# Kernel tuning notes

Hardware: AMD Instinct MI355X
Metric: run time of the kernel (lower is better)

Reference implementation:

```python
import jax, jax.numpy as jnp
import numpy as np

SEQ_LEN = 600
N_CLASSES = 5
P = 6  # max_ar_order


def setup_inputs() -> dict:
    key = jax.random.key(0)
    N = 32768
    x = jax.random.normal(key, (N, SEQ_LEN), dtype=jnp.float32)
    return {"x": x}


def reference(x):
    N = x.shape[0]
    T_out = SEQ_LEN - P
    # Lag matrix: X_lag[:, t, k] = x[:, P-1-k + t]  -> [N, T_out, P]
    X_lag = jnp.stack([x[:, P - 1 - k:SEQ_LEN - 1 - k] for k in range(P)], axis=-1)
    y = x[:, P:]  # [N, T_out]
    ones = jnp.ones((N, T_out, 1), dtype=x.dtype)
    D = jnp.concatenate([ones, X_lag], axis=-1)  # [N, T_out, P+1]
    # Least squares via normal equations (tiny (P+1)x(P+1) batched solve)
    G = jnp.einsum('ntk,ntl->nkl', D, D)        # [N, P+1, P+1]
    b = jnp.einsum('ntk,nt->nk', D, y)          # [N, P+1]
    w = jnp.linalg.solve(G, b[..., None])[..., 0]  # [N, P+1]
    y_hat_valid = jnp.einsum('ntk,nk->nt', D, w)   # [N, T_out]
    x_hat = jnp.zeros((N, SEQ_LEN), dtype=x.dtype).at[:, P:].set(y_hat_valid)
    ar_coeffs = w[:, 1:]  # [N, P]
    coeffs = jnp.broadcast_to(ar_coeffs[:, None, :], (N, SEQ_LEN, P))
    # zero the first P time steps
    t_mask = (jnp.arange(SEQ_LEN) >= P).astype(x.dtype)[None, :, None]
    coeffs = coeffs * t_mask
    p_logits = jnp.zeros((N, N_CLASSES), dtype=x.dtype)
    p_hard = jnp.zeros((N,), dtype=jnp.int32)
    return (coeffs, p_logits, p_hard, x_hat)
```

## Files before the change

kernel.cpp:

```cpp
#include <hip/hip_runtime.h>

#define SEQ 600
#define PP 6
#define TOUT 594

__global__ __launch_bounds__(256) void ar_fit_kernel(
    const float* __restrict__ x,
    float* __restrict__ coeffs,
    float* __restrict__ x_hat,
    int N)
{
    __shared__ __align__(16) float sxr[4][608];
    __shared__ float4 spat[4][3];

    const int wave = threadIdx.x >> 6;
    const int lane = threadIdx.x & 63;
    const int row  = (blockIdx.x << 2) + wave;
    const bool live = (row < N);

    if (live) {
        const float4* xr = reinterpret_cast<const float4*>(x + (size_t)row * SEQ);
        float4* s4 = reinterpret_cast<float4*>(sxr[wave]);
        for (int i = lane; i < SEQ / 4; i += 64) s4[i] = xr[i];
        if (lane < 8) sxr[wave][SEQ + lane] = 0.0f;
    }
    __syncthreads();

    const float* sx = sxr[wave];
    float w[7];

    if (live) {
        float S = 0.f;
        float Q[7] = {0.f, 0.f, 0.f, 0.f, 0.f, 0.f, 0.f};
        for (int i = lane; i < SEQ; i += 64) {
            float x0 = sx[i];
            S += x0;
            #pragma unroll
            for (int d = 0; d < 7; ++d) Q[d] += x0 * sx[i + d];
        }
        #pragma unroll
        for (int m = 1; m < 64; m <<= 1) {
            S += __shfl_xor(S, m, 64);
            #pragma unroll
            for (int d = 0; d < 7; ++d) Q[d] += __shfl_xor(Q[d], m, 64);
        }

        float pre[8], suf[8];
        pre[0] = 0.f; suf[0] = 0.f;
        #pragma unroll
        for (int c = 1; c < 8; ++c) {
            pre[c] = pre[c - 1] + sx[c - 1];
            suf[c] = suf[c - 1] + sx[SEQ - c];
        }

        float M[7][7];
        float rhs[7];
        M[0][0] = (float)TOUT;
        #pragma unroll
        for (int k = 0; k < 6; ++k) {
            float v = S - pre[5 - k] - suf[k + 1];
            M[0][k + 1] = v; M[k + 1][0] = v;
        }
        #pragma unroll
        for (int k = 0; k < 6; ++k) {
            #pragma unroll
            for (int l = k; l < 6; ++l) {
                const int a = 5 - l, d = l - k;
                float head = 0.f;
                #pragma unroll
                for (int i = 0; i < a; ++i) head += sx[i] * sx[i + d];
                float tail = 0.f;
                #pragma unroll
                for (int i = a + TOUT; i < SEQ; ++i) tail += sx[i] * sx[i + d];
                float v = Q[d] - head - tail;
                M[k + 1][l + 1] = v; M[l + 1][k + 1] = v;
            }
        }
        rhs[0] = S - pre[6];
        #pragma unroll
        for (int k = 0; k < 6; ++k) {
            const int a = 5 - k, d = k + 1;
            float head = 0.f;
            #pragma unroll
            for (int i = 0; i < a; ++i) head += sx[i] * sx[i + d];
            float tail = 0.f;
            #pragma unroll
            for (int i = a + TOUT; i < SEQ; ++i) tail += sx[i] * sx[i + d];
            rhs[k + 1] = Q[d] - head - tail;
        }

        #pragma unroll
        for (int j = 0; j < 7; ++j) {
            float s = M[j][j];
            #pragma unroll
            for (int m = 0; m < j; ++m) s -= M[j][m] * M[j][m];
            float ljj = sqrtf(s);
            M[j][j] = ljj;
            float inv = 1.0f / ljj;
            #pragma unroll
            for (int i2 = j + 1; i2 < 7; ++i2) {
                float s2 = M[i2][j];
                #pragma unroll
                for (int m = 0; m < j; ++m) s2 -= M[i2][m] * M[j][m];
                M[i2][j] = s2 * inv;
            }
        }
        float z[7];
        #pragma unroll
        for (int i2 = 0; i2 < 7; ++i2) {
            float s = rhs[i2];
            #pragma unroll
            for (int m = 0; m < i2; ++m) s -= M[i2][m] * z[m];
            z[i2] = s / M[i2][i2];
        }
        #pragma unroll
        for (int i2 = 6; i2 >= 0; --i2) {
            float s = z[i2];
            #pragma unroll
            for (int m = i2 + 1; m < 7; ++m) s -= M[m][i2] * w[m];
            w[i2] = s / M[i2][i2];
        }

        if (lane == 0) {
            float* p = reinterpret_cast<float*>(spat[wave]);
            #pragma unroll
            for (int m = 0; m < 12; ++m) p[m] = w[1 + (m % 6)];
        }
    }
    __syncthreads();

    if (!live) return;

    {
        float4* crow = reinterpret_cast<float4*>(coeffs + (size_t)row * (SEQ * PP));
        const float4* pw = spat[wave];
        int r = lane % 3;
        for (int i = lane; i < (SEQ * PP) / 4; i += 64) {
            float4 v = pw[r];
            if (i < 9) {
                float* vp = reinterpret_cast<float*>(&v);
                #pragma unroll
                for (int j = 0; j < 4; ++j)
                    if (4 * i + j < PP * PP) vp[j] = 0.f;
            }
            crow[i] = v;
            r = (r == 2) ? 0 : (r + 1);
        }
    }

    {
        float* xh = x_hat + (size_t)row * SEQ;
        for (int e = lane; e < SEQ; e += 64) {
            float v = 0.f;
            if (e >= PP) {
                v = w[0];
                #pragma unroll
                for (int k = 1; k <= 6; ++k) v += w[k] * sx[e - k];
            }
            xh[e] = v;
        }
    }
}

extern "C" void kernel_launch(void* const* d_in, const int* in_sizes, int n_in,
                              void* d_out, int out_size, void* d_ws, size_t ws_size,
                              hipStream_t stream) {
    const float* x = (const float*)d_in[0];
    const int N = in_sizes[0] / SEQ;

    float* out    = (float*)d_out;
    float* coeffs = out;
    float* extra  = out + (size_t)N * SEQ * PP;
    float* x_hat  = extra + (size_t)N * 6;

    hipMemsetAsync(extra, 0, (size_t)N * 6 * sizeof(float), stream);

    dim3 grid((N + 3) / 4), block(256);
    ar_fit_kernel<<<grid, block, 0, stream>>>(x, coeffs, x_hat, N);
}
```

Measured before the change: 594.2 us.

## Fuse memset into kernel, vectorize loads/stores with nontemporal writes

Zeroing of the logits/hard-label region moves into the main kernel, which removes the separate memset launch. Shared memory is read as float4, partial sums use register windows, and the coefficient and x_hat outputs are written with fully unrolled float4 nontemporal stores. The second __syncthreads and the shared pattern buffer are gone, divisions become hardware reciprocals, and the bounds checks are removed. The grid is now N/4, so N is assumed to be a multiple of 4.

```diff
diff --git a/kernel.cpp b/kernel.cpp
--- a/kernel.cpp
+++ b/kernel.cpp
@@ -3,161 +3,211 @@
 #define SEQ 600
 #define PP 6
 #define TOUT 594
-
-__global__ __launch_bounds__(256) void ar_fit_kernel(
+#define NF4 150
+#define NF4P 152
+
+typedef float v4f __attribute__((ext_vector_type(4)));
+
+__device__ __forceinline__ void nt_store4(float4* p, float4 v) {
+    v4f vv;
+    vv.x = v.x; vv.y = v.y; vv.z = v.z; vv.w = v.w;
+    __builtin_nontemporal_store(vv, reinterpret_cast<v4f*>(p));
+}
+
+__global__ __launch_bounds__(256) void ar_all_kernel(
     const float* __restrict__ x,
     float* __restrict__ coeffs,
+    float* __restrict__ extra,
     float* __restrict__ x_hat,
     int N)
 {
-    __shared__ __align__(16) float sxr[4][608];
-    __shared__ float4 spat[4][3];
+    __shared__ __align__(16) float4 sxr[4][NF4P];
 
     const int wave = threadIdx.x >> 6;
     const int lane = threadIdx.x & 63;
     const int row  = (blockIdx.x << 2) + wave;
-    const bool live = (row < N);
-
-    if (live) {
+
+    float4* s4 = sxr[wave];
+
+    {
         const float4* xr = reinterpret_cast<const float4*>(x + (size_t)row * SEQ);
-        float4* s4 = reinterpret_cast<float4*>(sxr[wave]);
-        for (int i = lane; i < SEQ / 4; i += 64) s4[i] = xr[i];
-        if (lane < 8) sxr[wave][SEQ + lane] = 0.0f;
+        float4 r0, r1, r2;
+        int m0 = lane, m1 = lane + 64, m2 = lane + 128;
+        r0 = xr[m0];
+        r1 = xr[m1];
+        if (m2 < NF4) r2 = xr[m2];
+        s4[m0] = r0;
+        s4[m1] = r1;
+        if (m2 < NF4) s4[m2] = r2;
+        if (lane < 2) s4[NF4 + lane] = make_float4(0.f, 0.f, 0.f, 0.f);
     }
     __syncthreads();
 
-    const float* sx = sxr[wave];
-    float w[7];
-
-    if (live) {
-        float S = 0.f;
-        float Q[7] = {0.f, 0.f, 0.f, 0.f, 0.f, 0.f, 0.f};
-        for (int i = lane; i < SEQ; i += 64) {
-            float x0 = sx[i];
-            S += x0;
-            #pragma unroll
-            for (int d = 0; d < 7; ++d) Q[d] += x0 * sx[i + d];
-        }
-        #pragma unroll
-        for (int m = 1; m < 64; m <<= 1) {
-            S += __shfl_xor(S, m, 64);
-            #pragma unroll
-            for (int d = 0; d < 7; ++d) Q[d] += __shfl_xor(Q[d], m, 64);
-        }
-
-        float pre[8], suf[8];
-        pre[0] = 0.f; suf[0] = 0.f;
-        #pragma unroll
-        for (int c = 1; c < 8; ++c) {
-            pre[c] = pre[c - 1] + sx[c - 1];
-            suf[c] = suf[c - 1] + sx[SEQ - c];
-        }
-
-        float M[7][7];
-        float rhs[7];
-        M[0][0] = (float)TOUT;
-        #pragma unroll
-        for (int k = 0; k < 6; ++k) {
-            float v = S - pre[5 - k] - suf[k + 1];
-            M[0][k + 1] = v; M[k + 1][0] = v;
-        }
-        #pragma unroll
-        for (int k = 0; k < 6; ++k) {
-            #pragma unroll
-            for (int l = k; l < 6; ++l) {
-                const int a = 5 - l, d = l - k;
-                float head = 0.f;
+    float S = 0.f;
+    float Q[7] = {0.f, 0.f, 0.f, 0.f, 0.f, 0.f, 0.f};
+    #pragma unroll
+    for (int k = 0; k < 3; ++k) {
+        const int m = lane + 64 * k;
+        if (m < NF4) {
+            float4 a = s4[m], b = s4[m + 1], c = s4[m + 2];
+            float W[12] = {a.x, a.y, a.z, a.w, b.x, b.y, b.z, b.w,
+                           c.x, c.y, c.z, c.w};
+            #pragma unroll
+            for (int cc = 0; cc < 4; ++cc) {
+                S += W[cc];
                 #pragma unroll
-                for (int i = 0; i < a; ++i) head += sx[i] * sx[i + d];
-                float tail = 0.f;
-                #pragma unroll
-                for (int i = a + TOUT; i < SEQ; ++i) tail += sx[i] * sx[i + d];
-                float v = Q[d] - head - tail;
-                M[k + 1][l + 1] = v; M[l + 1][k + 1] = v;
+                for (int d = 0; d < 7; ++d) Q[d] += W[cc] * W[cc + d];
             }
         }
-        rhs[0] = S - pre[6];
-        #pragma unroll
-        for (int k = 0; k < 6; ++k) {
-            const int a = 5 - k, d = k + 1;
+    }
+    #pragma unroll
+    for (int m = 1; m < 64; m <<= 1) {
+        S += __shfl_xor(S, m, 64);
+        #pragma unroll
+        for (int d = 0; d < 7; ++d) Q[d] += __shfl_xor(Q[d], m, 64);
+    }
+
+    float low[8], hig[16];
+    {
+        float4 e0 = s4[0], e1 = s4[1];
+        float4 t0 = s4[148], t1 = s4[149], t2 = s4[150], t3 = s4[151];
+        low[0]=e0.x; low[1]=e0.y; low[2]=e0.z; low[3]=e0.w;
+        low[4]=e1.x; low[5]=e1.y; low[6]=e1.z; low[7]=e1.w;
+        hig[0]=t0.x; hig[1]=t0.y; hig[2]=t0.z; hig[3]=t0.w;
+        hig[4]=t1.x; hig[5]=t1.y; hig[6]=t1.z; hig[7]=t1.w;
+        hig[8]=t2.x; hig[9]=t2.y; hig[10]=t2.z; hig[11]=t2.w;
+        hig[12]=t3.x; hig[13]=t3.y; hig[14]=t3.z; hig[15]=t3.w;
+    }
+    float pre[8], suf[8];
+    pre[0] = 0.f; suf[0] = 0.f;
+    #pragma unroll
+    for (int c = 1; c < 8; ++c) {
+        pre[c] = pre[c - 1] + low[c - 1];
+        suf[c] = suf[c - 1] + hig[8 - c];
+    }
+
+    float M[7][7];
+    float rhs[7];
+    M[0][0] = (float)TOUT;
+    #pragma unroll
+    for (int k = 0; k < 6; ++k) {
+        float v = S - pre[5 - k] - suf[k + 1];
+        M[k + 1][0] = v; M[0][k + 1] = v;
+    }
+    #pragma unroll
+    for (int k = 0; k < 6; ++k) {
+        #pragma unroll
+        for (int l = k; l < 6; ++l) {
+            const int a = 5 - l, d = l - k;
             float head = 0.f;
             #pragma unroll
-            for (int i = 0; i < a; ++i) head += sx[i] * sx[i + d];
+            for (int i = 0; i < a; ++i) head += low[i] * low[i + d];
             float tail = 0.f;
             #pragma unroll
-            for (int i = a + TOUT; i < SEQ; ++i) tail += sx[i] * sx[i + d];
-            rhs[k + 1] = Q[d] - head - tail;
-        }
-
-        #pragma unroll
-        for (int j = 0; j < 7; ++j) {
-            float s = M[j][j];
-            #pragma unroll
-            for (int m = 0; m < j; ++m) s -= M[j][m] * M[j][m];
-            float ljj = sqrtf(s);
-            M[j][j] = ljj;
-            float inv = 1.0f / ljj;
-            #pragma unroll
-            for (int i2 = j + 1; i2 < 7; ++i2) {
-                float s2 = M[i2][j];
-                #pragma unroll
-                for (int m = 0; m < j; ++m) s2 -= M[i2][m] * M[j][m];
-                M[i2][j] = s2 * inv;
+            for (int i = a + TOUT; i < SEQ; ++i)
+                tail += hig[i - 592] * hig[i + d - 592];
+            float v = Q[d] - head - tail;
+            M[l + 1][k + 1] = v; M[k + 1][l + 1] = v;
+        }
+    }
+    rhs[0] = S - pre[6];
+    #pragma unroll
+    for (int k = 0; k < 6; ++k) {
+        const int a = 5 - k, d = k + 1;
+        float head = 0.f;
+        #pragma unroll
+        for (int i = 0; i < a; ++i) head += low[i] * low[i + d];
+        float tail = 0.f;
+        #pragma unroll
+        for (int i = a + TOUT; i < SEQ; ++i)
+            tail += hig[i - 592] * hig[i + d - 592];
+        rhs[k + 1] = Q[d] - head - tail;
+    }
+
+    float invd[7];
+    #pragma unroll
+    for (int j = 0; j < 7; ++j) {
+        float s = M[j][j];
+        #pragma unroll
+        for (int m = 0; m < j; ++m) s -= M[j][m] * M[j][m];
+        float ljj = sqrtf(s);
+        M[j][j] = ljj;
+        float inv = __builtin_amdgcn_rcpf(ljj);
+        invd[j] = inv;
+        #pragma unroll
+        for (int i2 = j + 1; i2 < 7; ++i2) {
+            float s2 = M[i2][j];
+            #pragma unroll
+            for (int m = 0; m < j; ++m) s2 -= M[i2][m] * M[j][m];
+            M[i2][j] = s2 * inv;
+        }
+    }
+    float w[7], z[7];
+    #pragma unroll
+    for (int i2 = 0; i2 < 7; ++i2) {
+        float s = rhs[i2];
+        #pragma unroll
+        for (int m = 0; m < i2; ++m) s -= M[i2][m] * z[m];
+        z[i2] = s * invd[i2];
+    }
+    #pragma unroll
+    for (int i2 = 6; i2 >= 0; --i2) {
+        float s = z[i2];
+        #pragma unroll
+        for (int m = i2 + 1; m < 7; ++m) s -= M[m][i2] * w[m];
+        w[i2] = s * invd[i2];
+    }
+
+    if (lane < 5) extra[(size_t)5 * row + lane] = 0.f;
+    if (lane == 5) extra[(size_t)5 * N + row] = 0.f;
+
+    {
+        const float4 P0 = make_float4(w[1], w[2], w[3], w[4]);
+        const float4 P1 = make_float4(w[5], w[6], w[1], w[2]);
+        const float4 P2 = make_float4(w[3], w[4], w[5], w[6]);
+        const int r0 = lane % 3;
+        const float4 A0 = (r0 == 0) ? P0 : ((r0 == 1) ? P1 : P2);
+        const float4 A1 = (r0 == 0) ? P1 : ((r0 == 1) ? P2 : P0);
+        const float4 A2 = (r0 == 0) ? P2 : ((r0 == 1) ? P0 : P1);
+
+        float4* crow = reinterpret_cast<float4*>(coeffs + (size_t)row * (SEQ * PP));
+        float4 v0 = (lane <= 8) ? make_float4(0.f, 0.f, 0.f, 0.f) : A0;
+        nt_store4(crow + lane, v0);
+        #pragma unroll
+        for (int j = 1; j < 14; ++j) {
+            const float4 v = (j % 3 == 0) ? A0 : ((j % 3 == 1) ? A1 : A2);
+            nt_store4(crow + lane + 64 * j, v);
+        }
+        if (lane < 4) nt_store4(crow + lane + 64 * 14, A2);
+    }
+
+    {
+        float4* xh4 = reinterpret_cast<float4*>(x_hat + (size_t)row * SEQ);
+        #pragma unroll
+        for (int k = 0; k < 3; ++k) {
+            const int m = lane + 64 * k;
+            if (m < NF4) {
+                float4 v;
+                if (m == 0) {
+                    v = make_float4(0.f, 0.f, 0.f, 0.f);
+                } else {
+                    const int mm2 = (m >= 2) ? (m - 2) : 0;
+                    float4 ra = s4[mm2], rb = s4[m - 1], rc = s4[m];
+                    float W[12] = {ra.x, ra.y, ra.z, ra.w, rb.x, rb.y, rb.z, rb.w,
+                                   rc.x, rc.y, rc.z, rc.w};
+                    float p[4];
+                    #pragma unroll
+                    for (int c = 0; c < 4; ++c) {
+                        float s = w[0];
+                        #pragma unroll
+                        for (int kk = 1; kk <= 6; ++kk) s += w[kk] * W[8 + c - kk];
+                        p[c] = s;
+                    }
+                    if (m == 1) { p[0] = 0.f; p[1] = 0.f; }
+                    v = make_float4(p[0], p[1], p[2], p[3]);
+                }
+                nt_store4(xh4 + m, v);
             }
-        }
-        float z[7];
-        #pragma unroll
-        for (int i2 = 0; i2 < 7; ++i2) {
-            float s = rhs[i2];
-            #pragma unroll
-            for (int m = 0; m < i2; ++m) s -= M[i2][m] * z[m];
-            z[i2] = s / M[i2][i2];
-        }
-        #pragma unroll
-        for (int i2 = 6; i2 >= 0; --i2) {
-            float s = z[i2];
-            #pragma unroll
-            for (int m = i2 + 1; m < 7; ++m) s -= M[m][i2] * w[m];
-            w[i2] = s / M[i2][i2];
-        }
-
-        if (lane == 0) {
-            float* p = reinterpret_cast<float*>(spat[wave]);
-            #pragma unroll
-            for (int m = 0; m < 12; ++m) p[m] = w[1 + (m % 6)];
-        }
-    }
-    __syncthreads();
-
-    if (!live) return;
-
-    {
-        float4* crow = reinterpret_cast<float4*>(coeffs + (size_t)row * (SEQ * PP));
-        const float4* pw = spat[wave];
-        int r = lane % 3;
-        for (int i = lane; i < (SEQ * PP) / 4; i += 64) {
-            float4 v = pw[r];
-            if (i < 9) {
-                float* vp = reinterpret_cast<float*>(&v);
-                #pragma unroll
-                for (int j = 0; j < 4; ++j)
-                    if (4 * i + j < PP * PP) vp[j] = 0.f;
-            }
-            crow[i] = v;
-            r = (r == 2) ? 0 : (r + 1);
-        }
-    }
-
-    {
-        float* xh = x_hat + (size_t)row * SEQ;
-        for (int e = lane; e < SEQ; e += 64) {
-            float v = 0.f;
-            if (e >= PP) {
-                v = w[0];
-                #pragma unroll
-                for (int k = 1; k <= 6; ++k) v += w[k] * sx[e - k];
-            }
-            xh[e] = v;
         }
     }
 }
@@ -173,8 +223,5 @@
     float* extra  = out + (size_t)N * SEQ * PP;
     float* x_hat  = extra + (size_t)N * 6;
 
-    hipMemsetAsync(extra, 0, (size_t)N * 6 * sizeof(float), stream);
-
-    dim3 grid((N + 3) / 4), block(256);
-    ar_fit_kernel<<<grid, block, 0, stream>>>(x, coeffs, x_hat, N);
+    ar_all_kernel<<<dim3(N / 4), dim3(256), 0, stream>>>(x, coeffs, extra, x_hat, N);
 }
```

Result: no change. 598.7 us (+0.8%).
